# Performance work log

Measured on AMD Instinct MI355X. Metric: run time of the kernel, lower is better.

The kernel has to match this reference:

```python
import jax, jax.numpy as jnp
import numpy as np

S, B, I, H = 2048, 4096, 2, 6  # seq, batch, input_size, hidden_size


def setup_inputs() -> dict:
    key = jax.random.key(0)
    ks = jax.random.split(key, 11)
    init = lambda k, sh: jax.random.normal(k, sh, dtype=jnp.float32) * 0.1
    return {
        "x": jax.random.normal(ks[0], (S, B, I), dtype=jnp.float32),
        # layer-0 LSTM params (PyTorch gate order: i, f, g, o)
        "Wih0": init(ks[1], (4 * H, I)),
        "Whh0": init(ks[2], (4 * H, H)),
        "bih0": init(ks[3], (4 * H,)),
        "bhh0": init(ks[4], (4 * H,)),
        # layer-1 LSTM params
        "Wih1": init(ks[5], (4 * H, H)),
        "Whh1": init(ks[6], (4 * H, H)),
        "bih1": init(ks[7], (4 * H,)),
        "bhh1": init(ks[8], (4 * H,)),
        # final Linear(6, 1)
        "W2": init(ks[9], (1, H)),
        "b2": init(ks[10], (1,)),
    }


def _lstm_layer(x, Wih, Whh, bih, bhh):
    # x: (S, B, in_dim) -> hidden outputs (S, B, H)
    Bn = x.shape[1]
    Hn = Whh.shape[1]
    b = bih + bhh
    # precompute input projections for all timesteps at once (memory-bound GEMM)
    xg = jnp.einsum("sbi,gi->sbg", x, Wih) + b  # (S, B, 4H)

    def step(carry, xt_g):
        h, c = carry
        g = xt_g + h @ Whh.T  # (B, 4H)
        i, f, gg, o = jnp.split(g, 4, axis=-1)
        i = jax.nn.sigmoid(i)
        f = jax.nn.sigmoid(f)
        gg = jnp.tanh(gg)
        o = jax.nn.sigmoid(o)
        c = f * c + i * gg
        h = o * jnp.tanh(c)
        return (h, c), h

    h0 = jnp.zeros((Bn, Hn), dtype=x.dtype)
    c0 = jnp.zeros((Bn, Hn), dtype=x.dtype)
    _, hs = jax.lax.scan(step, (h0, c0), xg)
    return hs  # (S, B, H)


def reference(x, Wih0, Whh0, bih0, bhh0, Wih1, Whh1, bih1, bhh1, W2, b2):
    h1 = _lstm_layer(x, Wih0, Whh0, bih0, bhh0)   # (S, B, H)
    h2 = _lstm_layer(h1, Wih1, Whh1, bih1, bhh1)  # (S, B, H); dropout disabled (eval)
    flat = h2.reshape(-1, H)                       # (S*B, H)
    out = flat @ W2.T + b2                         # (S*B, 1) — original discards final view
    return out
```

## Files before the change

kernel.cpp:

```cpp
#include <hip/hip_runtime.h>

#define SEQ   2048
#define BATCH 4096
#define HID   6

typedef float v2 __attribute__((ext_vector_type(2)));

__device__ __forceinline__ float fexp2(float a) {
#if __has_builtin(__builtin_amdgcn_exp2f)
  return __builtin_amdgcn_exp2f(a);
#else
  float r; asm("v_exp_f32 %0, %1" : "=v"(r) : "v"(a)); return r;
#endif
}
__device__ __forceinline__ float frcp(float a) {
#if __has_builtin(__builtin_amdgcn_rcpf)
  return __builtin_amdgcn_rcpf(a);
#else
  float r; asm("v_rcp_f32 %0, %1" : "=v"(r) : "v"(a)); return r;
#endif
}

template <int CTRL>
__device__ __forceinline__ float dppf(float v) {
  int r = __builtin_amdgcn_update_dpp(0, __builtin_bit_cast(int, v), CTRL, 0xF, 0xF, true);
  return __builtin_bit_cast(float, r);
}

__global__ __launch_bounds__(64, 1) void lstm2_kernel(
    const float* __restrict__ x,
    const float* __restrict__ Wih0, const float* __restrict__ Whh0,
    const float* __restrict__ bih0, const float* __restrict__ bhh0,
    const float* __restrict__ Wih1, const float* __restrict__ Whh1,
    const float* __restrict__ bih1, const float* __restrict__ bhh1,
    const float* __restrict__ W2,   const float* __restrict__ b2,
    float* __restrict__ out)
{
  const int tid = blockIdx.x * 64 + threadIdx.x;
  const int b   = tid >> 4;
  const int l   = threadIdx.x & 15;
  const int u   = l & 7;
  const int p   = (l >> 3) & 1;
  const int uu  = (u < HID) ? u : (HID - 1);
  const int r0  = p ? (2 * HID + uu) : uu;
  const int r1  = p ? (3 * HID + uu) : (HID + uu);

  v2 wh0a2[4], wh0b2[4], wi1a2[4], wi1b2[4], wh1a2[4], wh1b2[4], w2r2[4];
#pragma unroll
  for (int k = 0; k < 4; ++k) {
    const int k0 = u ^ (2 * k), k1 = u ^ (2 * k + 1);
    const bool ok0 = (k0 < HID), ok1 = (k1 < HID);
    wh0a2[k] = v2{ok0 ? Whh0[r0 * HID + k0] : 0.f, ok1 ? Whh0[r0 * HID + k1] : 0.f};
    wh0b2[k] = v2{ok0 ? Whh0[r1 * HID + k0] : 0.f, ok1 ? Whh0[r1 * HID + k1] : 0.f};
    wi1a2[k] = v2{ok0 ? Wih1[r0 * HID + k0] : 0.f, ok1 ? Wih1[r0 * HID + k1] : 0.f};
    wi1b2[k] = v2{ok0 ? Wih1[r1 * HID + k0] : 0.f, ok1 ? Wih1[r1 * HID + k1] : 0.f};
    wh1a2[k] = v2{ok0 ? Whh1[r0 * HID + k0] : 0.f, ok1 ? Whh1[r0 * HID + k1] : 0.f};
    wh1b2[k] = v2{ok0 ? Whh1[r1 * HID + k0] : 0.f, ok1 ? Whh1[r1 * HID + k1] : 0.f};
    w2r2[k]  = v2{ok0 ? W2[k0] : 0.f,             ok1 ? W2[k1] : 0.f};
  }
  const v2 wx0p = v2{Wih0[r0 * 2 + 0], Wih0[r0 * 2 + 1]};
  const v2 wx1p = v2{Wih0[r1 * 2 + 0], Wih0[r1 * 2 + 1]};
  const v2 B0A = v2{bih0[r0] + bhh0[r0], 0.f};
  const v2 B0B = v2{bih0[r1] + bhh0[r1], 0.f};
  const v2 B1A = v2{bih1[r0] + bhh1[r0], 0.f};
  const v2 B1B = v2{bih1[r1] + bhh1[r1], 0.f};
  const float bout = b2[0];

  const float A  = p ? 2.f : 1.f;
  const float Bc = p ? -1.f : 0.f;
  const float K0 = -1.4426950408889634f * A;
  const float KS = -1.4426950408889634f;
  const float KT =  2.8853900817779268f;

  float c0 = 0.f, c1 = 0.f;
  float h0p = 0.f, h1p = 0.f;
  v2 h0g[4], h1g[4];

  auto actupd = [&](float a0, float a1, float& c) -> float {
    float g0 = fmaf(A, frcp(1.f + fexp2(a0 * K0)), Bc);
    float g1 = frcp(1.f + fexp2(a1 * KS));
    float xg0 = dppf<0x128>(g0);
    float xg1 = dppf<0x128>(g1);
    float m = g0 * xg0;
    float f = p ? xg1 : g1;
    float o = p ? g1  : xg1;
    c = fmaf(f, c, m);
    float t = fmaf(-2.f, frcp(1.f + fexp2(c * KT)), 1.f);
    return o * t;
  };

  auto gath = [&](float h, v2 (&g)[4]) {
    float t1 = dppf<0xB1>(h);
    float t2 = dppf<0x4E>(h);
    float t3 = dppf<0x4E>(t1);
    g[0] = v2{h, t1};
    g[1] = v2{t2, t3};
    g[2] = v2{dppf<0x124>(h),  dppf<0x124>(t1)};
    g[3] = v2{dppf<0x124>(t2), dppf<0x124>(t3)};
  };

  auto dot8 = [](const v2 (&w)[4], const v2 (&g)[4], v2 acc) -> v2 {
#pragma unroll
    for (int k = 0; k < 4; ++k) acc = __builtin_elementwise_fma(w[k], g[k], acc);
    return acc;
  };

  const v2* x2 = (const v2*)x;
  v2 xc  = x2[(size_t)0 * BATCH + b];
  v2 xn1 = x2[(size_t)1 * BATCH + b];
  v2 xn2 = x2[(size_t)2 * BATCH + b];
  v2 xn3 = x2[(size_t)3 * BATCH + b];

  {
    v2 A0 = __builtin_elementwise_fma(wx0p, xc, B0A);
    v2 A1 = __builtin_elementwise_fma(wx1p, xc, B0B);
    h0p = actupd(A0.x + A0.y, A1.x + A1.y, c0);
    v2 xf = x2[(size_t)4 * BATCH + b];
    xc = xn1; xn1 = xn2; xn2 = xn3; xn3 = xf;
  }

#pragma unroll 1
  for (int t = 1; t < SEQ; ++t) {
    int tf = t + 4; tf = (tf < SEQ) ? tf : (SEQ - 1);
    v2 xf = x2[(size_t)tf * BATCH + b];

    gath(h0p, h0g);
    gath(h1p, h1g);

    v2 A00 = dot8(wh0a2, h0g, __builtin_elementwise_fma(wx0p, xc, B0A));
    v2 A01 = dot8(wh0b2, h0g, __builtin_elementwise_fma(wx1p, xc, B0B));
    v2 A10 = dot8(wh1a2, h1g, dot8(wi1a2, h0g, B1A));
    v2 A11 = dot8(wh1b2, h1g, dot8(wi1b2, h0g, B1B));

    if (t >= 2) {
      v2 AO = dot8(w2r2, h1g, v2{bout, 0.f});
      if (l == 0) out[(size_t)(t - 2) * BATCH + b] = AO.x + AO.y;
    }

    float h0c = actupd(A00.x + A00.y, A01.x + A01.y, c0);
    float h1c = actupd(A10.x + A10.y, A11.x + A11.y, c1);

    h0p = h0c; h1p = h1c;
    xc = xn1; xn1 = xn2; xn2 = xn3; xn3 = xf;
  }

  {
    gath(h0p, h0g);
    gath(h1p, h1g);
    {
      v2 AO = dot8(w2r2, h1g, v2{bout, 0.f});
      if (l == 0) out[(size_t)(SEQ - 2) * BATCH + b] = AO.x + AO.y;
    }
    v2 A10 = dot8(wh1a2, h1g, dot8(wi1a2, h0g, B1A));
    v2 A11 = dot8(wh1b2, h1g, dot8(wi1b2, h0g, B1B));
    float h1c = actupd(A10.x + A10.y, A11.x + A11.y, c1);
    gath(h1c, h1g);
    v2 AO = dot8(w2r2, h1g, v2{bout, 0.f});
    if (l == 0) out[(size_t)(SEQ - 1) * BATCH + b] = AO.x + AO.y;
  }
}

extern "C" void kernel_launch(void* const* d_in, const int* in_sizes, int n_in,
                              void* d_out, int out_size, void* d_ws, size_t ws_size,
                              hipStream_t stream) {
  const float* x    = (const float*)d_in[0];
  const float* Wih0 = (const float*)d_in[1];
  const float* Whh0 = (const float*)d_in[2];
  const float* bih0 = (const float*)d_in[3];
  const float* bhh0 = (const float*)d_in[4];
  const float* Wih1 = (const float*)d_in[5];
  const float* Whh1 = (const float*)d_in[6];
  const float* bih1 = (const float*)d_in[7];
  const float* bhh1 = (const float*)d_in[8];
  const float* W2   = (const float*)d_in[9];
  const float* b2   = (const float*)d_in[10];
  float* out = (float*)d_out;

  dim3 grid(BATCH * 16 / 64);
  dim3 block(64);
  hipLaunchKernelGGL(lstm2_kernel, grid, block, 0, stream,
                     x, Wih0, Whh0, bih0, bhh0, Wih1, Whh1, bih1, bhh1, W2, b2, out);
}
```

Baseline: 731.1 us.

## Buffer outputs in shared memory and flush coalesced rows every 64 steps

Blocks grow from 64 to 256 threads so each block covers 16 batch elements. Per-step scalar output stores, which were scattered single-float writes, are staged in a 64x16 LDS buffer and written out as coalesced float4 rows once every 64 timesteps. The cost is two block-wide barriers per flush, which couple four wavefronts that previously ran independently through the latency-bound recurrence, and a grid with a quarter as many blocks.

```diff
diff --git a/kernel.cpp b/kernel.cpp
--- a/kernel.cpp
+++ b/kernel.cpp
@@ -3,6 +3,7 @@
 #define SEQ   2048
 #define BATCH 4096
 #define HID   6
+#define BLK   256
 
 typedef float v2 __attribute__((ext_vector_type(2)));
 
@@ -27,7 +28,7 @@
   return __builtin_bit_cast(float, r);
 }
 
-__global__ __launch_bounds__(64, 1) void lstm2_kernel(
+__global__ __launch_bounds__(BLK, 1) void lstm2_kernel(
     const float* __restrict__ x,
     const float* __restrict__ Wih0, const float* __restrict__ Whh0,
     const float* __restrict__ bih0, const float* __restrict__ bhh0,
@@ -36,14 +37,17 @@
     const float* __restrict__ W2,   const float* __restrict__ b2,
     float* __restrict__ out)
 {
-  const int tid = blockIdx.x * 64 + threadIdx.x;
-  const int b   = tid >> 4;
-  const int l   = threadIdx.x & 15;
-  const int u   = l & 7;
-  const int p   = (l >> 3) & 1;
-  const int uu  = (u < HID) ? u : (HID - 1);
-  const int r0  = p ? (2 * HID + uu) : uu;
-  const int r1  = p ? (3 * HID + uu) : (HID + uu);
+  __shared__ float obuf[64][16];
+
+  const int tidb = threadIdx.x;
+  const int g    = tidb >> 4;
+  const int b    = blockIdx.x * 16 + g;
+  const int l    = tidb & 15;
+  const int u    = l & 7;
+  const int p    = (l >> 3) & 1;
+  const int uu   = (u < HID) ? u : (HID - 1);
+  const int r0   = p ? (2 * HID + uu) : uu;
+  const int r1   = p ? (3 * HID + uu) : (HID + uu);
 
   v2 wh0a2[4], wh0b2[4], wi1a2[4], wi1b2[4], wh1a2[4], wh1b2[4], w2r2[4];
 #pragma unroll
@@ -105,6 +109,12 @@
     return acc;
   };
 
+  auto flush = [&](int rbase) {
+    const int row = tidb >> 2, j = tidb & 3;
+    float4 vv = *(const float4*)&obuf[row][j * 4];
+    *(float4*)&out[(size_t)(rbase + row) * BATCH + blockIdx.x * 16 + j * 4] = vv;
+  };
+
   const v2* x2 = (const v2*)x;
   v2 xc  = x2[(size_t)0 * BATCH + b];
   v2 xn1 = x2[(size_t)1 * BATCH + b];
@@ -133,8 +143,14 @@
     v2 A11 = dot8(wh1b2, h1g, dot8(wi1b2, h0g, B1B));
 
     if (t >= 2) {
+      const int r = t - 2;
       v2 AO = dot8(w2r2, h1g, v2{bout, 0.f});
-      if (l == 0) out[(size_t)(t - 2) * BATCH + b] = AO.x + AO.y;
+      if (l == 0) obuf[r & 63][g] = AO.x + AO.y;
+      if ((r & 63) == 63) {
+        __syncthreads();
+        flush(r - 63);
+        __syncthreads();
+      }
     }
 
     float h0c = actupd(A00.x + A00.y, A01.x + A01.y, c0);
@@ -149,14 +165,16 @@
     gath(h1p, h1g);
     {
       v2 AO = dot8(w2r2, h1g, v2{bout, 0.f});
-      if (l == 0) out[(size_t)(SEQ - 2) * BATCH + b] = AO.x + AO.y;
+      if (l == 0) obuf[62][g] = AO.x + AO.y;
     }
     v2 A10 = dot8(wh1a2, h1g, dot8(wi1a2, h0g, B1A));
     v2 A11 = dot8(wh1b2, h1g, dot8(wi1b2, h0g, B1B));
     float h1c = actupd(A10.x + A10.y, A11.x + A11.y, c1);
     gath(h1c, h1g);
     v2 AO = dot8(w2r2, h1g, v2{bout, 0.f});
-    if (l == 0) out[(size_t)(SEQ - 1) * BATCH + b] = AO.x + AO.y;
+    if (l == 0) obuf[63][g] = AO.x + AO.y;
+    __syncthreads();
+    flush(SEQ - 64);
   }
 }
 
@@ -176,8 +194,8 @@
   const float* b2   = (const float*)d_in[10];
   float* out = (float*)d_out;
 
-  dim3 grid(BATCH * 16 / 64);
-  dim3 block(64);
+  dim3 grid(BATCH * 16 / BLK);
+  dim3 block(BLK);
   hipLaunchKernelGGL(lstm2_kernel, grid, block, 0, stream,
                      x, Wih0, Whh0, bih0, bhh0, Wih1, Whh1, bih1, bhh1, W2, b2, out);
 }
```

New measurement: 697.7 us. 1.05x faster.
